# Kernel optimization log

Measured on AMD Instinct MI355X. Metric: run time of the kernel, lower is better.

The kernel has to match this reference:

```python
import math
import jax, jax.numpy as jnp
import numpy as np

B, S, IN_DIM = 4, 2048, 256
L, H, NHEAD, FFN = 3, 256, 4, 1024
CF, CB = 32, 32  # context_forward / context_backward window
EPS = 1e-5


def sinusoidal_pe(seq_len, d_model):
    pos = jnp.arange(seq_len, dtype=jnp.float32)[:, None]
    div = jnp.exp(jnp.arange(0, d_model, 2, dtype=jnp.float32) * (-math.log(10000.0) / d_model))
    pe = jnp.zeros((seq_len, d_model), dtype=jnp.float32)
    pe = pe.at[:, 0::2].set(jnp.sin(pos * div))
    pe = pe.at[:, 1::2].set(jnp.cos(pos * div))
    return pe


def band_mask(s):
    # True = allowed: -CB <= j - i <= CF (sliding window, from triu/transpose construction)
    i = jnp.arange(s)[:, None]
    j = jnp.arange(s)[None, :]
    return (j - i <= CF) & (i - j <= CB)


def layer_norm(x, g, b):
    mu = jnp.mean(x, axis=-1, keepdims=True)
    var = jnp.mean((x - mu) ** 2, axis=-1, keepdims=True)
    return (x - mu) * jax.lax.rsqrt(var + EPS) * g + b


def mha(x, wqkv, bqkv, wo, bo, mask):
    b, s, d = x.shape
    dh = d // NHEAD
    qkv = x @ wqkv.T + bqkv  # [b, s, 3d]
    q, k, v = jnp.split(qkv, 3, axis=-1)
    split = lambda t: t.reshape(b, s, NHEAD, dh).transpose(0, 2, 1, 3)  # [b, h, s, dh]
    q, k, v = split(q), split(k), split(v)
    scores = jnp.einsum('bhqd,bhkd->bhqk', q, k) / math.sqrt(dh)
    scores = jnp.where(mask, scores, -jnp.inf)
    attn = jax.nn.softmax(scores, axis=-1)
    o = jnp.einsum('bhqk,bhkd->bhqd', attn, v).transpose(0, 2, 1, 3).reshape(b, s, d)
    return o @ wo.T + bo


def setup_inputs() -> dict:
    key = jax.random.key(0)
    ks = jax.random.split(key, 12)
    sc = 0.02
    inp = {
        'x': jax.random.normal(ks[0], (B, S, IN_DIM), dtype=jnp.float32),
        'w_in': sc * jax.random.normal(ks[1], (H, IN_DIM), dtype=jnp.float32),
        'w_out': sc * jax.random.normal(ks[2], (IN_DIM, H), dtype=jnp.float32),
        'b_out': jnp.zeros((IN_DIM,), dtype=jnp.float32),
        'qkv_w': sc * jax.random.normal(ks[3], (L, 3 * H, H), dtype=jnp.float32),
        'qkv_b': jnp.zeros((L, 3 * H), dtype=jnp.float32),
        'out_w': sc * jax.random.normal(ks[4], (L, H, H), dtype=jnp.float32),
        'out_b': jnp.zeros((L, H), dtype=jnp.float32),
        'ln1_g': jnp.ones((L, H), dtype=jnp.float32),
        'ln1_b': jnp.zeros((L, H), dtype=jnp.float32),
        'ln2_g': jnp.ones((L, H), dtype=jnp.float32),
        'ln2_b': jnp.zeros((L, H), dtype=jnp.float32),
        'ff1_w': sc * jax.random.normal(ks[5], (L, FFN, H), dtype=jnp.float32),
        'ff1_b': jnp.zeros((L, FFN), dtype=jnp.float32),
        'ff2_w': sc * jax.random.normal(ks[6], (L, H, FFN), dtype=jnp.float32),
        'ff2_b': jnp.zeros((L, H), dtype=jnp.float32),
        'lnf_g': jnp.ones((H,), dtype=jnp.float32),
        'lnf_b': jnp.zeros((H,), dtype=jnp.float32),
    }
    return inp


def reference(x, w_in, w_out, b_out, qkv_w, qkv_b, out_w, out_b,
              ln1_g, ln1_b, ln2_g, ln2_b, ff1_w, ff1_b, ff2_w, ff2_b,
              lnf_g, lnf_b):
    b, s, _ = x.shape
    mask = band_mask(s)
    h = math.sqrt(H) * (x @ w_in.T) + sinusoidal_pe(s, H)[None]
    for l in range(L):  # pre-norm transformer encoder layers (relu FFN, eval/no-dropout)
        h = h + mha(layer_norm(h, ln1_g[l], ln1_b[l]), qkv_w[l], qkv_b[l], out_w[l], out_b[l], mask)
        z = layer_norm(h, ln2_g[l], ln2_b[l])
        h = h + (jax.nn.relu(z @ ff1_w[l].T + ff1_b[l]) @ ff2_w[l].T + ff2_b[l])
    h = layer_norm(h, lnf_g, lnf_b)
    return h @ w_out.T + b_out
```

## Files before the change

kernel.cpp:

```cpp
#include <hip/hip_runtime.h>
#include <hip/hip_bf16.h>
#include <math.h>

#define SEQ 2048
#define BATCH 4
#define HDIM 256
#define NHEAD 4
#define FFN_DIM 1024
#define MTOT (BATCH*SEQ)

typedef __attribute__((ext_vector_type(8))) short bf16x8;
typedef __attribute__((ext_vector_type(4))) float f32x4;

__device__ __forceinline__ bf16x8 cvt8(const float* p)
{
    float4 a = *(const float4*)p;
    float4 b = *(const float4*)(p + 4);
    union { bf16x8 v; __hip_bfloat16 e[8]; } u;
    u.e[0] = __float2bfloat16(a.x); u.e[1] = __float2bfloat16(a.y);
    u.e[2] = __float2bfloat16(a.z); u.e[3] = __float2bfloat16(a.w);
    u.e[4] = __float2bfloat16(b.x); u.e[5] = __float2bfloat16(b.y);
    u.e[6] = __float2bfloat16(b.z); u.e[7] = __float2bfloat16(b.w);
    return u.v;
}

__global__ __launch_bounds__(256)
void cvt_all(const float* __restrict__ w_in, const float* __restrict__ w_out,
             const float* __restrict__ qkv_w, const float* __restrict__ out_w,
             const float* __restrict__ ff1_w, const float* __restrict__ ff2_w,
             __hip_bfloat16* __restrict__ wb)
{
    int i = blockIdx.x * 256 + threadIdx.x;
    size_t e = (size_t)i * 8;

    const float* srcbase; size_t rbase; int kshift;
    if (e < 720896) {
        if (e < 65536)       { srcbase = w_in;  rbase = 0;      kshift = 8; }
        else if (e < 131072) { srcbase = w_out; rbase = 65536;  kshift = 8; }
        else                 { srcbase = qkv_w; rbase = 131072; kshift = 8; }
    } else if (e < 917504)   { srcbase = out_w; rbase = 720896; kshift = 8; }
    else if (e < 1703936)    { srcbase = ff1_w; rbase = 917504; kshift = 8; }
    else                     { srcbase = ff2_w; rbase = 1703936; kshift = 10; }

    size_t local = e - rbase;
    int K = 1 << kshift;
    int row = (int)(local >> kshift);
    int k   = (int)(local & (K - 1));

    size_t dst = rbase
               + ((size_t)(row >> 4) * (K >> 5) + (k >> 5)) * 512
               + (size_t)((((k >> 3) & 3) << 4) | (row & 15)) * 8;

    *(bf16x8*)(wb + dst) = cvt8(srcbase + local);
}

__device__ __forceinline__ bf16x8 fragW(const short* W, int n0, int k0, int K, int lane)
{
    return *(const bf16x8*)(W + ((size_t)(n0 >> 4) * (K >> 5) + (k0 >> 5)) * 512 + lane * 8);
}

__global__ __launch_bounds__(256)
void embed_pe(const float* __restrict__ X, const __hip_bfloat16* __restrict__ W,
              float* __restrict__ hbuf)
{
    int tid = threadIdx.x, wave = tid >> 6, lane = tid & 63;
    int wm = wave >> 1, wn = wave & 1;
    int rowBase = blockIdx.y * 64 + wm * 32;
    int colBase = blockIdx.x * 64 + wn * 32;
    int lr = lane & 15, hi = lane >> 4;

    const float* px0 = X + (size_t)(rowBase + lr) * HDIM + hi * 8;
    const float* px1 = px0 + (size_t)16 * HDIM;
    const short* Wb  = (const short*)W;

    f32x4 acc[2][2];
    acc[0][0] = (f32x4){0.f,0.f,0.f,0.f}; acc[0][1] = (f32x4){0.f,0.f,0.f,0.f};
    acc[1][0] = (f32x4){0.f,0.f,0.f,0.f}; acc[1][1] = (f32x4){0.f,0.f,0.f,0.f};

    #pragma unroll
    for (int k0 = 0; k0 < 256; k0 += 32) {
        bf16x8 a0 = cvt8(px0 + k0);
        bf16x8 a1 = cvt8(px1 + k0);
        bf16x8 b0 = fragW(Wb, colBase,      k0, 256, lane);
        bf16x8 b1 = fragW(Wb, colBase + 16, k0, 256, lane);
        acc[0][0] = __builtin_amdgcn_mfma_f32_16x16x32_bf16(a0, b0, acc[0][0], 0,0,0);
        acc[0][1] = __builtin_amdgcn_mfma_f32_16x16x32_bf16(a0, b1, acc[0][1], 0,0,0);
        acc[1][0] = __builtin_amdgcn_mfma_f32_16x16x32_bf16(a1, b0, acc[1][0], 0,0,0);
        acc[1][1] = __builtin_amdgcn_mfma_f32_16x16x32_bf16(a1, b1, acc[1][1], 0,0,0);
    }

    int cc = lane & 15, quad = lane >> 4;
    #pragma unroll
    for (int mt = 0; mt < 2; mt++)
        #pragma unroll
        for (int nt = 0; nt < 2; nt++) {
            int col = colBase + nt*16 + cc;
            int i2 = col & ~1;
            float freq = __expf((float)i2 * (-9.210340371976184f / 256.0f));
            #pragma unroll
            for (int r = 0; r < 4; r++) {
                int row = rowBase + mt*16 + quad*4 + r;
                float arg = (float)(row & (SEQ-1)) * freq;
                float pe = (col & 1) ? __cosf(arg) : __sinf(arg);
                hbuf[(size_t)row*HDIM + col] = 16.0f*acc[mt][nt][r] + pe;
            }
        }
}

template<int MODE, int NT>
__global__ __launch_bounds__(256)
void gemm_ln(const float* __restrict__ h,
             const float* __restrict__ g, const float* __restrict__ bln,
             const __hip_bfloat16* __restrict__ W,
             const float* __restrict__ bias,
             __hip_bfloat16* __restrict__ obf, float* __restrict__ of32,
             int N, int ldw)
{
    constexpr int NTW = NT / 32;
    __shared__ __align__(16) short A_lds[64][264];

    int tid = threadIdx.x, wave = tid >> 6, lane = tid & 63;
    int wm = wave >> 1, wn = wave & 1;
    int rowBase = blockIdx.y * 64;
    int colBase = blockIdx.x * NT + wn * (NT / 2);

    {
        float4 gv = *(const float4*)(g + lane * 4);
        float4 bv = *(const float4*)(bln + lane * 4);
        #pragma unroll
        for (int rr = 0; rr < 16; rr += 4) {
            float4 xv[4];
            #pragma unroll
            for (int u = 0; u < 4; u++)
                xv[u] = *(const float4*)(h + (size_t)(rowBase + wave*16 + rr + u)*HDIM + lane*4);
            #pragma unroll
            for (int u = 0; u < 4; u++) {
                float s = xv[u].x + xv[u].y + xv[u].z + xv[u].w;
                #pragma unroll
                for (int off = 32; off >= 1; off >>= 1) s += __shfl_xor(s, off);
                float mu = s * (1.0f/256.0f);
                float d0 = xv[u].x-mu, d1 = xv[u].y-mu, d2 = xv[u].z-mu, d3 = xv[u].w-mu;
                float v = d0*d0 + d1*d1 + d2*d2 + d3*d3;
                #pragma unroll
                for (int off = 32; off >= 1; off >>= 1) v += __shfl_xor(v, off);
                float rstd = rsqrtf(v * (1.0f/256.0f) + 1e-5f);
                union { short e[4]; uint2 w2; } o;
                o.e[0] = (short)__bfloat16_as_ushort(__float2bfloat16(d0*rstd*gv.x + bv.x));
                o.e[1] = (short)__bfloat16_as_ushort(__float2bfloat16(d1*rstd*gv.y + bv.y));
                o.e[2] = (short)__bfloat16_as_ushort(__float2bfloat16(d2*rstd*gv.z + bv.z));
                o.e[3] = (short)__bfloat16_as_ushort(__float2bfloat16(d3*rstd*gv.w + bv.w));
                *(uint2*)&A_lds[wave*16 + rr + u][lane*4] = o.w2;
            }
        }
    }
    __syncthreads();

    int lr = lane & 15, hi = lane >> 4;
    f32x4 acc[2][NTW];
    #pragma unroll
    for (int mt = 0; mt < 2; mt++)
        #pragma unroll
        for (int nt = 0; nt < NTW; nt++)
            acc[mt][nt] = (f32x4){0.f,0.f,0.f,0.f};

    const short* Ws = (const short*)W;
    #pragma unroll
    for (int k0 = 0; k0 < 256; k0 += 32) {
        bf16x8 af[2], bfr[NTW];
        #pragma unroll
        for (int mt = 0; mt < 2; mt++)
            af[mt] = *(const bf16x8*)&A_lds[wm*32 + mt*16 + lr][k0 + hi*8];
        #pragma unroll
        for (int nt = 0; nt < NTW; nt++)
            bfr[nt] = fragW(Ws, colBase + nt*16, k0, 256, lane);
        #pragma unroll
        for (int mt = 0; mt < 2; mt++)
            #pragma unroll
            for (int nt = 0; nt < NTW; nt++)
                acc[mt][nt] = __builtin_amdgcn_mfma_f32_16x16x32_bf16(af[mt], bfr[nt], acc[mt][nt], 0,0,0);
    }

    int cc = lane & 15, quad = lane >> 4;
    #pragma unroll
    for (int mt = 0; mt < 2; mt++)
        #pragma unroll
        for (int nt = 0; nt < NTW; nt++) {
            int col = colBase + nt*16 + cc;
            float bv = bias[col];
            #pragma unroll
            for (int r = 0; r < 4; r++) {
                int row = rowBase + wm*32 + mt*16 + quad*4 + r;
                float c = acc[mt][nt][r] + bv;
                if (MODE == 4) { of32[(size_t)row*N + col] = c; }
                else {
                    int sec = col >> 8, hd = (col >> 6) & 3, d = col & 63;
                    int srow = row & (SEQ - 1);
                    size_t base = (size_t)sec * 2097152
                                + (size_t)(((row >> 11) << 2) | hd) * 131072;
                    size_t idx;
                    if (sec < 2)
                        idx = base + (size_t)(srow >> 4) * 1024 + (size_t)(d >> 5) * 512
                            + (size_t)((((d >> 3) & 3) << 4) | (srow & 15)) * 8 + (d & 7);
                    else
                        idx = base + (size_t)srow * 64 + d;
                    obf[idx] = __float2bfloat16(c);
                }
            }
        }
}

struct AttnLDS {
    __align__(16) __hip_bfloat16 Vt[64][128];
    __align__(16) __hip_bfloat16 Pl[32][96];
    float sm[2][32], ss[2][32];
};

__global__ __launch_bounds__(1024)
void attn_ffn(const __hip_bfloat16* __restrict__ qkvd,
              const __hip_bfloat16* __restrict__ ow,
              const float* __restrict__ ob,
              float* __restrict__ h,
              const float* __restrict__ g, const float* __restrict__ bln,
              const __hip_bfloat16* __restrict__ W1, const float* __restrict__ b1,
              const __hip_bfloat16* __restrict__ W2, const float* __restrict__ b2)
{
    __shared__ union SMem {
        AttnLDS asl[4];
        struct {
            __align__(16) short A[32][264];
            __align__(16) short Z[2][32][264];
        } f;
    } U;
    __shared__ __align__(16) short att_lds[32][264];
    __shared__ __align__(16) float H_lds[32][260];

    int tid  = threadIdx.x;
    int wave = tid >> 6, lane = tid & 63;
    int grp  = wave >> 2, w4 = wave & 3, ltid = tid & 255;
    int b    = blockIdx.y, i0 = blockIdx.x * 32;
    int klo  = i0 - 32;

    int lr = lane & 15, hi = lane >> 4;
    int cc = lane & 15, quad = lane >> 4;

    int hd = grp;
    AttnLDS& S = U.asl[grp];
    const short* Qd = (const short*)qkvd + (size_t)(b * 4 + hd) * 131072;
    const short* Kd = Qd + 2097152;
    const short* Vd = Qd + 4194304;
    int qh = w4 & 1, seg = w4 >> 1;
    int qoff = qh * 16 + quad * 4;

    int vm = ltid & 7, vrl = ltid >> 3, vdp = vm * 8;
    bf16x8 vr[3];
    #pragma unroll
    for (int rr = 0; rr < 3; rr++) {
        int j = klo + rr * 32 + vrl;
        j = j < 0 ? 0 : (j > SEQ - 1 ? SEQ - 1 : j);
        vr[rr] = *(const bf16x8*)(Vd + (size_t)j * 64 + vdp);
    }
    bf16x8 qf[2];
    #pragma unroll
    for (int ds = 0; ds < 2; ds++)
        qf[ds] = *(const bf16x8*)(Qd + (size_t)((i0 >> 4) + qh) * 1024 + ds * 512 + lane * 8);
    bf16x8 kf[3][2];
    #pragma unroll
    for (int t = 0; t < 3; t++) {
        int jt = (klo + seg * 48 + t * 16) >> 4;
        jt = jt < 0 ? 0 : (jt > 127 ? 127 : jt);
        kf[t][0] = *(const bf16x8*)(Kd + (size_t)jt * 1024 + lane * 8);
        kf[t][1] = *(const bf16x8*)(Kd + (size_t)jt * 1024 + 512 + lane * 8);
    }
    float hold[2][4];
    {
        const float* hp = h + (size_t)(b * SEQ + i0) * HDIM + wave * 16 + cc;
        #pragma unroll
        for (int mt = 0; mt < 2; mt++)
            #pragma unroll
            for (int r = 0; r < 4; r++)
                hold[mt][r] = hp[(size_t)(mt*16 + quad*4 + r) * HDIM];
    }

    {
        union { bf16x8 v; short e[8]; } u;
        #pragma unroll
        for (int rr = 0; rr < 3; rr++) {
            int row = rr * 32 + vrl;
            int colp = row ^ (vm << 3);
            u.v = vr[rr];
            #pragma unroll
            for (int jj = 0; jj < 8; jj++)
                *(short*)&S.Vt[vdp + jj][colp] = u.e[jj];
        }
    }

    f32x4 sacc[3];
    #pragma unroll
    for (int t = 0; t < 3; t++) {
        f32x4 a = (f32x4){0.f,0.f,0.f,0.f};
        a = __builtin_amdgcn_mfma_f32_16x16x32_bf16(qf[0], kf[t][0], a, 0,0,0);
        a = __builtin_amdgcn_mfma_f32_16x16x32_bf16(qf[1], kf[t][1], a, 0,0,0);
        sacc[t] = a;
    }

    float s[3][4];
    #pragma unroll
    for (int t = 0; t < 3; t++) {
        int koff = seg * 48 + t * 16 + cc;
        int jj = klo + koff;
        #pragma unroll
        for (int r = 0; r < 4; r++) {
            int rel = koff - (qoff + r);
            bool ok = (jj >= 0) && (jj < SEQ) && (rel >= 0) && (rel <= 64);
            s[t][r] = ok ? sacc[t][r] * 0.125f : -1e30f;
        }
    }

    float mrow[4], srow[4];
    #pragma unroll
    for (int r = 0; r < 4; r++)
        mrow[r] = fmaxf(fmaxf(s[0][r], s[1][r]), s[2][r]);
    #pragma unroll
    for (int off = 8; off >= 1; off >>= 1)
        #pragma unroll
        for (int r = 0; r < 4; r++)
            mrow[r] = fmaxf(mrow[r], __shfl_xor(mrow[r], off));
    #pragma unroll
    for (int r = 0; r < 4; r++)
        srow[r] = __expf(s[0][r]-mrow[r]) + __expf(s[1][r]-mrow[r]) + __expf(s[2][r]-mrow[r]);
    #pragma unroll
    for (int off = 8; off >= 1; off >>= 1)
        #pragma unroll
        for (int r = 0; r < 4; r++)
            srow[r] += __shfl_xor(srow[r], off);
    if (cc == 0) {
        #pragma unroll
        for (int r = 0; r < 4; r++) { S.sm[seg][qoff+r] = mrow[r]; S.ss[seg][qoff+r] = srow[r]; }
    }
    __syncthreads();

    float Mr[4], inv[4];
    #pragma unroll
    for (int r = 0; r < 4; r++) {
        float m0 = S.sm[0][qoff+r], m1 = S.sm[1][qoff+r];
        float M = fmaxf(m0, m1);
        float dn = S.ss[0][qoff+r] * __expf(m0 - M) + S.ss[1][qoff+r] * __expf(m1 - M);
        Mr[r] = M; inv[r] = 1.0f / dn;
    }
    #pragma unroll
    for (int t = 0; t < 3; t++)
        #pragma unroll
        for (int r = 0; r < 4; r++)
            S.Pl[qoff+r][seg*48 + t*16 + cc] = __float2bfloat16(__expf(s[t][r]-Mr[r]) * inv[r]);
    __syncthreads();

    bf16x8 owf[8];
    {
        const short* op = (const short*)ow + (size_t)wave * 8 * 512 + lane * 8;
        #pragma unroll
        for (int i = 0; i < 8; i++)
            owf[i] = *(const bf16x8*)(op + i * 512);
    }

    {
        f32x4 oacc[2];
        oacc[0] = (f32x4){0.f,0.f,0.f,0.f}; oacc[1] = (f32x4){0.f,0.f,0.f,0.f};
        #pragma unroll
        for (int ks = 0; ks < 3; ks++) {
            int kk = ks * 32;
            bf16x8 pf = *(const bf16x8*)&S.Pl[qh*16 + lr][kk + hi*8];
            #pragma unroll
            for (int dt = 0; dt < 2; dt++) {
                int d = seg*32 + dt*16 + lr;
                int colb = (kk + hi*8) ^ (((d >> 3) & 7) << 3);
                bf16x8 vf = *(const bf16x8*)&S.Vt[d][colb];
                oacc[dt] = __builtin_amdgcn_mfma_f32_16x16x32_bf16(pf, vf, oacc[dt], 0,0,0);
            }
        }
        #pragma unroll
        for (int dt = 0; dt < 2; dt++) {
            int col = hd*64 + seg*32 + dt*16 + cc;
            #pragma unroll
            for (int r = 0; r < 4; r++)
                att_lds[qoff + r][col] =
                    (short)__bfloat16_as_ushort(__float2bfloat16(oacc[dt][r]));
        }
    }
    __syncthreads();

    {
        f32x4 acc[2];
        acc[0] = (f32x4){0.f,0.f,0.f,0.f}; acc[1] = (f32x4){0.f,0.f,0.f,0.f};
        #pragma unroll
        for (int i = 0; i < 8; i++) {
            bf16x8 a0 = *(const bf16x8*)&att_lds[lr][i*32 + hi*8];
            bf16x8 a1 = *(const bf16x8*)&att_lds[16 + lr][i*32 + hi*8];
            acc[0] = __builtin_amdgcn_mfma_f32_16x16x32_bf16(a0, owf[i], acc[0], 0,0,0);
            acc[1] = __builtin_amdgcn_mfma_f32_16x16x32_bf16(a1, owf[i], acc[1], 0,0,0);
        }
        float bv = ob[wave*16 + cc];
        #pragma unroll
        for (int mt = 0; mt < 2; mt++)
            #pragma unroll
            for (int r = 0; r < 4; r++)
                H_lds[mt*16 + quad*4 + r][wave*16 + cc] = hold[mt][r] + acc[mt][r] + bv;
    }

    const short* W1s = (const short*)W1;
    const short* W2s = (const short*)W2;
    bf16x8 w1f[8];
    {
        const short* wp = W1s + (size_t)wave * 8 * 512 + lane * 8;
        #pragma unroll
        for (int i = 0; i < 8; i++)
            w1f[i] = *(const bf16x8*)(wp + i * 512);
    }
    __syncthreads();

    {
        float4 gv = *(const float4*)(g + lane * 4);
        float4 bv = *(const float4*)(bln + lane * 4);
        #pragma unroll
        for (int u = 0; u < 2; u++) {
            float4 xv = *(const float4*)&H_lds[wave*2 + u][lane*4];
            float ss2 = xv.x + xv.y + xv.z + xv.w;
            #pragma unroll
            for (int off = 32; off >= 1; off >>= 1) ss2 += __shfl_xor(ss2, off);
            float mu = ss2 * (1.0f/256.0f);
            float d0 = xv.x-mu, d1 = xv.y-mu, d2 = xv.z-mu, d3 = xv.w-mu;
            float v = d0*d0 + d1*d1 + d2*d2 + d3*d3;
            #pragma unroll
            for (int off = 32; off >= 1; off >>= 1) v += __shfl_xor(v, off);
            float rstd = rsqrtf(v * (1.0f/256.0f) + 1e-5f);
            union { short e[4]; uint2 w2; } o;
            o.e[0] = (short)__bfloat16_as_ushort(__float2bfloat16(d0*rstd*gv.x + bv.x));
            o.e[1] = (short)__bfloat16_as_ushort(__float2bfloat16(d1*rstd*gv.y + bv.y));
            o.e[2] = (short)__bfloat16_as_ushort(__float2bfloat16(d2*rstd*gv.z + bv.z));
            o.e[3] = (short)__bfloat16_as_ushort(__float2bfloat16(d3*rstd*gv.w + bv.w));
            *(uint2*)&U.f.A[wave*2 + u][lane*4] = o.w2;
        }
    }
    __syncthreads();

    f32x4 acc2[2];
    acc2[0] = (f32x4){0.f,0.f,0.f,0.f}; acc2[1] = (f32x4){0.f,0.f,0.f,0.f};

    #pragma unroll 1
    for (int kk = 0; kk < 4; kk++) {
        bf16x8 w2f[8];
        {
            const short* wp = W2s + (size_t)(wave * 32 + kk * 8) * 512 + lane * 8;
            #pragma unroll
            for (int i = 0; i < 8; i++)
                w2f[i] = *(const bf16x8*)(wp + i * 512);
        }

        f32x4 acc1[2];
        acc1[0] = (f32x4){0.f,0.f,0.f,0.f}; acc1[1] = (f32x4){0.f,0.f,0.f,0.f};
        #pragma unroll
        for (int i = 0; i < 8; i++) {
            bf16x8 af0 = *(const bf16x8*)&U.f.A[lr][i*32 + hi*8];
            bf16x8 af1 = *(const bf16x8*)&U.f.A[16 + lr][i*32 + hi*8];
            acc1[0] = __builtin_amdgcn_mfma_f32_16x16x32_bf16(af0, w1f[i], acc1[0], 0,0,0);
            acc1[1] = __builtin_amdgcn_mfma_f32_16x16x32_bf16(af1, w1f[i], acc1[1], 0,0,0);
        }

        {
            int col = wave*16 + cc;
            float bb = b1[kk*256 + col];
            #pragma unroll
            for (int mt = 0; mt < 2; mt++)
                #pragma unroll
                for (int r = 0; r < 4; r++) {
                    float z = fmaxf(acc1[mt][r] + bb, 0.f);
                    U.f.Z[kk & 1][mt*16 + quad*4 + r][col] =
                        (short)__bfloat16_as_ushort(__float2bfloat16(z));
                }
        }
        __syncthreads();

        {
            int nk = (kk < 3) ? kk + 1 : 3;
            const short* wp = W1s + (size_t)(nk * 16 + wave) * 8 * 512 + lane * 8;
            #pragma unroll
            for (int i = 0; i < 8; i++)
                w1f[i] = *(const bf16x8*)(wp + i * 512);
        }

        #pragma unroll
        for (int i = 0; i < 8; i++) {
            bf16x8 zf0 = *(const bf16x8*)&U.f.Z[kk & 1][lr][i*32 + hi*8];
            bf16x8 zf1 = *(const bf16x8*)&U.f.Z[kk & 1][16 + lr][i*32 + hi*8];
            acc2[0] = __builtin_amdgcn_mfma_f32_16x16x32_bf16(zf0, w2f[i], acc2[0], 0,0,0);
            acc2[1] = __builtin_amdgcn_mfma_f32_16x16x32_bf16(zf1, w2f[i], acc2[1], 0,0,0);
        }
    }

    {
        int col = wave*16 + cc;
        float bb = b2[col];
        #pragma unroll
        for (int mt = 0; mt < 2; mt++)
            #pragma unroll
            for (int r = 0; r < 4; r++) {
                int rowl = mt*16 + quad*4 + r;
                int row = b * SEQ + i0 + rowl;
                h[(size_t)row * HDIM + col] = H_lds[rowl][col] + acc2[mt][r] + bb;
            }
    }
}

extern "C" void kernel_launch(void* const* d_in, const int* in_sizes, int n_in,
                              void* d_out, int out_size, void* d_ws, size_t ws_size,
                              hipStream_t stream)
{
    const float* x     = (const float*)d_in[0];
    const float* w_in  = (const float*)d_in[1];
    const float* w_out = (const float*)d_in[2];
    const float* b_out = (const float*)d_in[3];
    const float* qkv_w = (const float*)d_in[4];
    const float* qkv_b = (const float*)d_in[5];
    const float* out_w = (const float*)d_in[6];
    const float* out_b = (const float*)d_in[7];
    const float* ln1_g = (const float*)d_in[8];
    const float* ln1_b = (const float*)d_in[9];
    const float* ln2_g = (const float*)d_in[10];
    const float* ln2_b = (const float*)d_in[11];
    const float* ff1_w = (const float*)d_in[12];
    const float* ff1_b = (const float*)d_in[13];
    const float* ff2_w = (const float*)d_in[14];
    const float* ff2_b = (const float*)d_in[15];
    const float* lnf_g = (const float*)d_in[16];
    const float* lnf_b = (const float*)d_in[17];

    char* ws = (char*)d_ws;
    float*          h    = (float*)ws;
    __hip_bfloat16* qkvd = (__hip_bfloat16*)(ws + 8388608);
    __hip_bfloat16* wb   = (__hip_bfloat16*)(ws + 25165824);

    __hip_bfloat16* w_in_b  = wb;
    __hip_bfloat16* w_out_b = wb + 65536;
    __hip_bfloat16* qkv_w_b = wb + 131072;
    __hip_bfloat16* out_w_b = wb + 720896;
    __hip_bfloat16* ff1_w_b = wb + 917504;
    __hip_bfloat16* ff2_w_b = wb + 1703936;

    dim3 blk(256);

    cvt_all<<<1216, blk, 0, stream>>>(w_in, w_out, qkv_w, out_w, ff1_w, ff2_w, wb);

    embed_pe<<<dim3(4, 128), blk, 0, stream>>>(x, w_in_b, h);

    for (int l = 0; l < 3; l++) {
        gemm_ln<5, 96><<<dim3(8, 128), blk, 0, stream>>>(
            h, ln1_g + l*HDIM, ln1_b + l*HDIM,
            qkv_w_b + (size_t)l*768*HDIM, qkv_b + l*768, qkvd, nullptr, 768, HDIM);
        attn_ffn<<<dim3(SEQ/32, BATCH), dim3(1024), 0, stream>>>(
            qkvd, out_w_b + (size_t)l*HDIM*HDIM, out_b + l*HDIM, h,
            ln2_g + l*HDIM, ln2_b + l*HDIM,
            ff1_w_b + (size_t)l*FFN_DIM*HDIM, ff1_b + l*FFN_DIM,
            ff2_w_b + (size_t)l*HDIM*FFN_DIM, ff2_b + l*HDIM);
    }

    gemm_ln<4, 64><<<dim3(4, 128), blk, 0, stream>>>(
        h, lnf_g, lnf_b, w_out_b, b_out, nullptr, (float*)d_out, HDIM, HDIM);
}
```

Measured before the change: 252.5 us.

## Fuse whole encoder into one cooperative persistent kernel with grid syncs

Replaces the embed, per-layer QKV GEMM, attention/FFN and final projection launches with one cooperative kernel. Each 32-row block keeps its residual stream in LDS for all layers, and grid.sync separates QKV production from the attention that reads neighbouring rows' K/V. QKV buffers are double-buffered so the next layer's QKV write does not overwrite data other blocks are still reading. This removes launch overhead and the global round trips of h. The cost is grid-wide barriers and a requirement that all 256 blocks of 1024 threads are co-resident.

```diff
diff --git a/kernel.cpp b/kernel.cpp
--- a/kernel.cpp
+++ b/kernel.cpp
@@ -1,6 +1,9 @@
 #include <hip/hip_runtime.h>
 #include <hip/hip_bf16.h>
+#include <hip/hip_cooperative_groups.h>
 #include <math.h>
+
+namespace cg = cooperative_groups;
 
 #define SEQ 2048
 #define BATCH 4
@@ -59,154 +62,44 @@
     return *(const bf16x8*)(W + ((size_t)(n0 >> 4) * (K >> 5) + (k0 >> 5)) * 512 + lane * 8);
 }
 
-__global__ __launch_bounds__(256)
-void embed_pe(const float* __restrict__ X, const __hip_bfloat16* __restrict__ W,
-              float* __restrict__ hbuf)
-{
-    int tid = threadIdx.x, wave = tid >> 6, lane = tid & 63;
-    int wm = wave >> 1, wn = wave & 1;
-    int rowBase = blockIdx.y * 64 + wm * 32;
-    int colBase = blockIdx.x * 64 + wn * 32;
-    int lr = lane & 15, hi = lane >> 4;
-
-    const float* px0 = X + (size_t)(rowBase + lr) * HDIM + hi * 8;
-    const float* px1 = px0 + (size_t)16 * HDIM;
-    const short* Wb  = (const short*)W;
-
-    f32x4 acc[2][2];
-    acc[0][0] = (f32x4){0.f,0.f,0.f,0.f}; acc[0][1] = (f32x4){0.f,0.f,0.f,0.f};
-    acc[1][0] = (f32x4){0.f,0.f,0.f,0.f}; acc[1][1] = (f32x4){0.f,0.f,0.f,0.f};
-
+__device__ __forceinline__ size_t qkv_idx(int row, int col)
+{
+    int sec = col >> 8, hd = (col >> 6) & 3, d = col & 63;
+    int srow = row & (SEQ - 1);
+    size_t base = (size_t)sec * 2097152
+                + (size_t)(((row >> 11) << 2) | hd) * 131072;
+    if (sec < 2)
+        return base + (size_t)(srow >> 4) * 1024 + (size_t)(d >> 5) * 512
+             + (size_t)((((d >> 3) & 3) << 4) | (srow & 15)) * 8 + (d & 7);
+    return base + (size_t)srow * 64 + d;
+}
+
+__device__ __forceinline__ void ln_rows(const float (*H)[260], short (*A)[264],
+                                        const float* __restrict__ g,
+                                        const float* __restrict__ bl,
+                                        int wave, int lane)
+{
+    float4 gv = *(const float4*)(g + lane * 4);
+    float4 bv = *(const float4*)(bl + lane * 4);
     #pragma unroll
-    for (int k0 = 0; k0 < 256; k0 += 32) {
-        bf16x8 a0 = cvt8(px0 + k0);
-        bf16x8 a1 = cvt8(px1 + k0);
-        bf16x8 b0 = fragW(Wb, colBase,      k0, 256, lane);
-        bf16x8 b1 = fragW(Wb, colBase + 16, k0, 256, lane);
-        acc[0][0] = __builtin_amdgcn_mfma_f32_16x16x32_bf16(a0, b0, acc[0][0], 0,0,0);
-        acc[0][1] = __builtin_amdgcn_mfma_f32_16x16x32_bf16(a0, b1, acc[0][1], 0,0,0);
-        acc[1][0] = __builtin_amdgcn_mfma_f32_16x16x32_bf16(a1, b0, acc[1][0], 0,0,0);
-        acc[1][1] = __builtin_amdgcn_mfma_f32_16x16x32_bf16(a1, b1, acc[1][1], 0,0,0);
+    for (int u = 0; u < 2; u++) {
+        float4 xv = *(const float4*)&H[wave*2 + u][lane*4];
+        float ss2 = xv.x + xv.y + xv.z + xv.w;
+        #pragma unroll
+        for (int off = 32; off >= 1; off >>= 1) ss2 += __shfl_xor(ss2, off);
+        float mu = ss2 * (1.0f/256.0f);
+        float d0 = xv.x-mu, d1 = xv.y-mu, d2 = xv.z-mu, d3 = xv.w-mu;
+        float v = d0*d0 + d1*d1 + d2*d2 + d3*d3;
+        #pragma unroll
+        for (int off = 32; off >= 1; off >>= 1) v += __shfl_xor(v, off);
+        float rstd = rsqrtf(v * (1.0f/256.0f) + 1e-5f);
+        union { short e[4]; uint2 w2; } o;
+        o.e[0] = (short)__bfloat16_as_ushort(__float2bfloat16(d0*rstd*gv.x + bv.x));
+        o.e[1] = (short)__bfloat16_as_ushort(__float2bfloat16(d1*rstd*gv.y + bv.y));
+        o.e[2] = (short)__bfloat16_as_ushort(__float2bfloat16(d2*rstd*gv.z + bv.z));
+        o.e[3] = (short)__bfloat16_as_ushort(__float2bfloat16(d3*rstd*gv.w + bv.w));
+        *(uint2*)&A[wave*2 + u][lane*4] = o.w2;
     }
-
-    int cc = lane & 15, quad = lane >> 4;
-    #pragma unroll
-    for (int mt = 0; mt < 2; mt++)
-        #pragma unroll
-        for (int nt = 0; nt < 2; nt++) {
-            int col = colBase + nt*16 + cc;
-            int i2 = col & ~1;
-            float freq = __expf((float)i2 * (-9.210340371976184f / 256.0f));
-            #pragma unroll
-            for (int r = 0; r < 4; r++) {
-                int row = rowBase + mt*16 + quad*4 + r;
-                float arg = (float)(row & (SEQ-1)) * freq;
-                float pe = (col & 1) ? __cosf(arg) : __sinf(arg);
-                hbuf[(size_t)row*HDIM + col] = 16.0f*acc[mt][nt][r] + pe;
-            }
-        }
-}
-
-template<int MODE, int NT>
-__global__ __launch_bounds__(256)
-void gemm_ln(const float* __restrict__ h,
-             const float* __restrict__ g, const float* __restrict__ bln,
-             const __hip_bfloat16* __restrict__ W,
-             const float* __restrict__ bias,
-             __hip_bfloat16* __restrict__ obf, float* __restrict__ of32,
-             int N, int ldw)
-{
-    constexpr int NTW = NT / 32;
-    __shared__ __align__(16) short A_lds[64][264];
-
-    int tid = threadIdx.x, wave = tid >> 6, lane = tid & 63;
-    int wm = wave >> 1, wn = wave & 1;
-    int rowBase = blockIdx.y * 64;
-    int colBase = blockIdx.x * NT + wn * (NT / 2);
-
-    {
-        float4 gv = *(const float4*)(g + lane * 4);
-        float4 bv = *(const float4*)(bln + lane * 4);
-        #pragma unroll
-        for (int rr = 0; rr < 16; rr += 4) {
-            float4 xv[4];
-            #pragma unroll
-            for (int u = 0; u < 4; u++)
-                xv[u] = *(const float4*)(h + (size_t)(rowBase + wave*16 + rr + u)*HDIM + lane*4);
-            #pragma unroll
-            for (int u = 0; u < 4; u++) {
-                float s = xv[u].x + xv[u].y + xv[u].z + xv[u].w;
-                #pragma unroll
-                for (int off = 32; off >= 1; off >>= 1) s += __shfl_xor(s, off);
-                float mu = s * (1.0f/256.0f);
-                float d0 = xv[u].x-mu, d1 = xv[u].y-mu, d2 = xv[u].z-mu, d3 = xv[u].w-mu;
-                float v = d0*d0 + d1*d1 + d2*d2 + d3*d3;
-                #pragma unroll
-                for (int off = 32; off >= 1; off >>= 1) v += __shfl_xor(v, off);
-                float rstd = rsqrtf(v * (1.0f/256.0f) + 1e-5f);
-                union { short e[4]; uint2 w2; } o;
-                o.e[0] = (short)__bfloat16_as_ushort(__float2bfloat16(d0*rstd*gv.x + bv.x));
-                o.e[1] = (short)__bfloat16_as_ushort(__float2bfloat16(d1*rstd*gv.y + bv.y));
-                o.e[2] = (short)__bfloat16_as_ushort(__float2bfloat16(d2*rstd*gv.z + bv.z));
-                o.e[3] = (short)__bfloat16_as_ushort(__float2bfloat16(d3*rstd*gv.w + bv.w));
-                *(uint2*)&A_lds[wave*16 + rr + u][lane*4] = o.w2;
-            }
-        }
-    }
-    __syncthreads();
-
-    int lr = lane & 15, hi = lane >> 4;
-    f32x4 acc[2][NTW];
-    #pragma unroll
-    for (int mt = 0; mt < 2; mt++)
-        #pragma unroll
-        for (int nt = 0; nt < NTW; nt++)
-            acc[mt][nt] = (f32x4){0.f,0.f,0.f,0.f};
-
-    const short* Ws = (const short*)W;
-    #pragma unroll
-    for (int k0 = 0; k0 < 256; k0 += 32) {
-        bf16x8 af[2], bfr[NTW];
-        #pragma unroll
-        for (int mt = 0; mt < 2; mt++)
-            af[mt] = *(const bf16x8*)&A_lds[wm*32 + mt*16 + lr][k0 + hi*8];
-        #pragma unroll
-        for (int nt = 0; nt < NTW; nt++)
-            bfr[nt] = fragW(Ws, colBase + nt*16, k0, 256, lane);
-        #pragma unroll
-        for (int mt = 0; mt < 2; mt++)
-            #pragma unroll
-            for (int nt = 0; nt < NTW; nt++)
-                acc[mt][nt] = __builtin_amdgcn_mfma_f32_16x16x32_bf16(af[mt], bfr[nt], acc[mt][nt], 0,0,0);
-    }
-
-    int cc = lane & 15, quad = lane >> 4;
-    #pragma unroll
-    for (int mt = 0; mt < 2; mt++)
-        #pragma unroll
-        for (int nt = 0; nt < NTW; nt++) {
-            int col = colBase + nt*16 + cc;
-            float bv = bias[col];
-            #pragma unroll
-            for (int r = 0; r < 4; r++) {
-                int row = rowBase + wm*32 + mt*16 + quad*4 + r;
-                float c = acc[mt][nt][r] + bv;
-                if (MODE == 4) { of32[(size_t)row*N + col] = c; }
-                else {
-                    int sec = col >> 8, hd = (col >> 6) & 3, d = col & 63;
-                    int srow = row & (SEQ - 1);
-                    size_t base = (size_t)sec * 2097152
-                                + (size_t)(((row >> 11) << 2) | hd) * 131072;
-                    size_t idx;
-                    if (sec < 2)
-                        idx = base + (size_t)(srow >> 4) * 1024 + (size_t)(d >> 5) * 512
-                            + (size_t)((((d >> 3) & 3) << 4) | (srow & 15)) * 8 + (d & 7);
-                    else
-                        idx = base + (size_t)srow * 64 + d;
-                    obf[idx] = __float2bfloat16(c);
-                }
-            }
-        }
 }
 
 struct AttnLDS {
@@ -216,13 +109,18 @@
 };
 
 __global__ __launch_bounds__(1024)
-void attn_ffn(const __hip_bfloat16* __restrict__ qkvd,
-              const __hip_bfloat16* __restrict__ ow,
-              const float* __restrict__ ob,
-              float* __restrict__ h,
-              const float* __restrict__ g, const float* __restrict__ bln,
-              const __hip_bfloat16* __restrict__ W1, const float* __restrict__ b1,
-              const __hip_bfloat16* __restrict__ W2, const float* __restrict__ b2)
+void mega(const float* __restrict__ X,
+          const __hip_bfloat16* __restrict__ wb,
+          const float* __restrict__ qkv_b,
+          const float* __restrict__ out_b,
+          const float* __restrict__ ln1_g, const float* __restrict__ ln1_b,
+          const float* __restrict__ ln2_g, const float* __restrict__ ln2_b,
+          const float* __restrict__ ff1_b, const float* __restrict__ ff2_b,
+          const float* __restrict__ lnf_g, const float* __restrict__ lnf_b,
+          const float* __restrict__ b_out,
+          float* __restrict__ outp,
+          __hip_bfloat16* __restrict__ qkvd0,
+          __hip_bfloat16* __restrict__ qkvd1)
 {
     __shared__ union SMem {
         AttnLDS asl[4];
@@ -234,6 +132,8 @@
     __shared__ __align__(16) short att_lds[32][264];
     __shared__ __align__(16) float H_lds[32][260];
 
+    cg::grid_group grid = cg::this_grid();
+
     int tid  = threadIdx.x;
     int wave = tid >> 6, lane = tid & 63;
     int grp  = wave >> 2, w4 = wave & 3, ltid = tid & 255;
@@ -242,271 +142,386 @@
 
     int lr = lane & 15, hi = lane >> 4;
     int cc = lane & 15, quad = lane >> 4;
-
-    int hd = grp;
-    AttnLDS& S = U.asl[grp];
-    const short* Qd = (const short*)qkvd + (size_t)(b * 4 + hd) * 131072;
-    const short* Kd = Qd + 2097152;
-    const short* Vd = Qd + 4194304;
     int qh = w4 & 1, seg = w4 >> 1;
     int qoff = qh * 16 + quad * 4;
 
-    int vm = ltid & 7, vrl = ltid >> 3, vdp = vm * 8;
-    bf16x8 vr[3];
-    #pragma unroll
-    for (int rr = 0; rr < 3; rr++) {
-        int j = klo + rr * 32 + vrl;
-        j = j < 0 ? 0 : (j > SEQ - 1 ? SEQ - 1 : j);
-        vr[rr] = *(const bf16x8*)(Vd + (size_t)j * 64 + vdp);
-    }
-    bf16x8 qf[2];
-    #pragma unroll
-    for (int ds = 0; ds < 2; ds++)
-        qf[ds] = *(const bf16x8*)(Qd + (size_t)((i0 >> 4) + qh) * 1024 + ds * 512 + lane * 8);
-    bf16x8 kf[3][2];
-    #pragma unroll
-    for (int t = 0; t < 3; t++) {
-        int jt = (klo + seg * 48 + t * 16) >> 4;
-        jt = jt < 0 ? 0 : (jt > 127 ? 127 : jt);
-        kf[t][0] = *(const bf16x8*)(Kd + (size_t)jt * 1024 + lane * 8);
-        kf[t][1] = *(const bf16x8*)(Kd + (size_t)jt * 1024 + 512 + lane * 8);
-    }
-    float hold[2][4];
+    const short* wbs = (const short*)wb;
+
     {
-        const float* hp = h + (size_t)(b * SEQ + i0) * HDIM + wave * 16 + cc;
+        const float* px0 = X + (size_t)(b*SEQ + i0 + lr) * HDIM + hi * 8;
+        const float* px1 = px0 + (size_t)16 * HDIM;
+        f32x4 acc[2];
+        acc[0] = (f32x4){0.f,0.f,0.f,0.f}; acc[1] = (f32x4){0.f,0.f,0.f,0.f};
+        #pragma unroll
+        for (int k0 = 0; k0 < 256; k0 += 32) {
+            bf16x8 a0 = cvt8(px0 + k0);
+            bf16x8 a1 = cvt8(px1 + k0);
+            bf16x8 b0 = fragW(wbs, wave*16, k0, 256, lane);
+            acc[0] = __builtin_amdgcn_mfma_f32_16x16x32_bf16(a0, b0, acc[0], 0,0,0);
+            acc[1] = __builtin_amdgcn_mfma_f32_16x16x32_bf16(a1, b0, acc[1], 0,0,0);
+        }
+        int col = wave*16 + cc;
+        int i2 = col & ~1;
+        float freq = __expf((float)i2 * (-9.210340371976184f / 256.0f));
         #pragma unroll
         for (int mt = 0; mt < 2; mt++)
             #pragma unroll
-            for (int r = 0; r < 4; r++)
-                hold[mt][r] = hp[(size_t)(mt*16 + quad*4 + r) * HDIM];
-    }
-
-    {
-        union { bf16x8 v; short e[8]; } u;
-        #pragma unroll
-        for (int rr = 0; rr < 3; rr++) {
-            int row = rr * 32 + vrl;
-            int colp = row ^ (vm << 3);
-            u.v = vr[rr];
-            #pragma unroll
-            for (int jj = 0; jj < 8; jj++)
-                *(short*)&S.Vt[vdp + jj][colp] = u.e[jj];
-        }
-    }
-
-    f32x4 sacc[3];
-    #pragma unroll
-    for (int t = 0; t < 3; t++) {
-        f32x4 a = (f32x4){0.f,0.f,0.f,0.f};
-        a = __builtin_amdgcn_mfma_f32_16x16x32_bf16(qf[0], kf[t][0], a, 0,0,0);
-        a = __builtin_amdgcn_mfma_f32_16x16x32_bf16(qf[1], kf[t][1], a, 0,0,0);
-        sacc[t] = a;
-    }
-
-    float s[3][4];
-    #pragma unroll
-    for (int t = 0; t < 3; t++) {
-        int koff = seg * 48 + t * 16 + cc;
-        int jj = klo + koff;
-        #pragma unroll
-        for (int r = 0; r < 4; r++) {
-            int rel = koff - (qoff + r);
-            bool ok = (jj >= 0) && (jj < SEQ) && (rel >= 0) && (rel <= 64);
-            s[t][r] = ok ? sacc[t][r] * 0.125f : -1e30f;
-        }
-    }
-
-    float mrow[4], srow[4];
-    #pragma unroll
-    for (int r = 0; r < 4; r++)
-        mrow[r] = fmaxf(fmaxf(s[0][r], s[1][r]), s[2][r]);
-    #pragma unroll
-    for (int off = 8; off >= 1; off >>= 1)
-        #pragma unroll
-        for (int r = 0; r < 4; r++)
-            mrow[r] = fmaxf(mrow[r], __shfl_xor(mrow[r], off));
-    #pragma unroll
-    for (int r = 0; r < 4; r++)
-        srow[r] = __expf(s[0][r]-mrow[r]) + __expf(s[1][r]-mrow[r]) + __expf(s[2][r]-mrow[r]);
-    #pragma unroll
-    for (int off = 8; off >= 1; off >>= 1)
-        #pragma unroll
-        for (int r = 0; r < 4; r++)
-            srow[r] += __shfl_xor(srow[r], off);
-    if (cc == 0) {
-        #pragma unroll
-        for (int r = 0; r < 4; r++) { S.sm[seg][qoff+r] = mrow[r]; S.ss[seg][qoff+r] = srow[r]; }
+            for (int r = 0; r < 4; r++) {
+                int srow = i0 + mt*16 + quad*4 + r;
+                float arg = (float)srow * freq;
+                float pe = (col & 1) ? __cosf(arg) : __sinf(arg);
+                H_lds[mt*16 + quad*4 + r][col] = 16.0f*acc[mt][r] + pe;
+            }
     }
     __syncthreads();
 
-    float Mr[4], inv[4];
-    #pragma unroll
-    for (int r = 0; r < 4; r++) {
-        float m0 = S.sm[0][qoff+r], m1 = S.sm[1][qoff+r];
-        float M = fmaxf(m0, m1);
-        float dn = S.ss[0][qoff+r] * __expf(m0 - M) + S.ss[1][qoff+r] * __expf(m1 - M);
-        Mr[r] = M; inv[r] = 1.0f / dn;
+    ln_rows(H_lds, U.f.A, ln1_g, ln1_b, wave, lane);
+    __syncthreads();
+    {
+        const short* Wts = wbs + 131072;
+        f32x4 qa[2][3];
+        #pragma unroll
+        for (int mt = 0; mt < 2; mt++)
+            #pragma unroll
+            for (int nt = 0; nt < 3; nt++)
+                qa[mt][nt] = (f32x4){0.f,0.f,0.f,0.f};
+        #pragma unroll
+        for (int k0 = 0; k0 < 256; k0 += 32) {
+            bf16x8 a0 = *(const bf16x8*)&U.f.A[lr][k0 + hi*8];
+            bf16x8 a1 = *(const bf16x8*)&U.f.A[16 + lr][k0 + hi*8];
+            #pragma unroll
+            for (int nt = 0; nt < 3; nt++) {
+                bf16x8 wf = fragW(Wts, wave*48 + nt*16, k0, 256, lane);
+                qa[0][nt] = __builtin_amdgcn_mfma_f32_16x16x32_bf16(a0, wf, qa[0][nt], 0,0,0);
+                qa[1][nt] = __builtin_amdgcn_mfma_f32_16x16x32_bf16(a1, wf, qa[1][nt], 0,0,0);
+            }
+        }
+        #pragma unroll
+        for (int nt = 0; nt < 3; nt++) {
+            int col = wave*48 + nt*16 + cc;
+            float bv = qkv_b[col];
+            #pragma unroll
+            for (int mt = 0; mt < 2; mt++)
+                #pragma unroll
+                for (int r = 0; r < 4; r++) {
+                    int row = b * SEQ + i0 + mt*16 + quad*4 + r;
+                    qkvd0[qkv_idx(row, col)] = __float2bfloat16(qa[mt][nt][r] + bv);
+                }
+        }
     }
-    #pragma unroll
-    for (int t = 0; t < 3; t++)
+    __threadfence();
+    grid.sync();
+
+    #pragma unroll 1
+    for (int l = 0; l < 3; l++) {
+        const short* Qbase = (const short*)((l == 1) ? qkvd1 : qkvd0);
+        const short* ows = wbs + 720896 + (size_t)l * 65536;
+        const short* W1s = wbs + 917504 + (size_t)l * 262144;
+        const short* W2s = wbs + 1703936 + (size_t)l * 262144;
+        const float* ob  = out_b + l * HDIM;
+        const float* b1  = ff1_b + l * FFN_DIM;
+        const float* b2  = ff2_b + l * HDIM;
+        const float* g2  = ln2_g + l * HDIM;
+        const float* bl2 = ln2_b + l * HDIM;
+
+        int hd = grp;
+        AttnLDS& S = U.asl[grp];
+        const short* Qd = Qbase + (size_t)(b * 4 + hd) * 131072;
+        const short* Kd = Qd + 2097152;
+        const short* Vd = Qd + 4194304;
+
+        int vm = ltid & 7, vrl = ltid >> 3, vdp = vm * 8;
+        bf16x8 vr[3];
+        #pragma unroll
+        for (int rr = 0; rr < 3; rr++) {
+            int j = klo + rr * 32 + vrl;
+            j = j < 0 ? 0 : (j > SEQ - 1 ? SEQ - 1 : j);
+            vr[rr] = *(const bf16x8*)(Vd + (size_t)j * 64 + vdp);
+        }
+        bf16x8 qf[2];
+        #pragma unroll
+        for (int ds = 0; ds < 2; ds++)
+            qf[ds] = *(const bf16x8*)(Qd + (size_t)((i0 >> 4) + qh) * 1024 + ds * 512 + lane * 8);
+        bf16x8 kf[3][2];
+        #pragma unroll
+        for (int t = 0; t < 3; t++) {
+            int jt = (klo + seg * 48 + t * 16) >> 4;
+            jt = jt < 0 ? 0 : (jt > 127 ? 127 : jt);
+            kf[t][0] = *(const bf16x8*)(Kd + (size_t)jt * 1024 + lane * 8);
+            kf[t][1] = *(const bf16x8*)(Kd + (size_t)jt * 1024 + 512 + lane * 8);
+        }
+
+        {
+            union { bf16x8 v; short e[8]; } u;
+            #pragma unroll
+            for (int rr = 0; rr < 3; rr++) {
+                int row = rr * 32 + vrl;
+                int colp = row ^ (vm << 3);
+                u.v = vr[rr];
+                #pragma unroll
+                for (int jj = 0; jj < 8; jj++)
+                    *(short*)&S.Vt[vdp + jj][colp] = u.e[jj];
+            }
+        }
+
+        f32x4 sacc[3];
+        #pragma unroll
+        for (int t = 0; t < 3; t++) {
+            f32x4 a = (f32x4){0.f,0.f,0.f,0.f};
+            a = __builtin_amdgcn_mfma_f32_16x16x32_bf16(qf[0], kf[t][0], a, 0,0,0);
+            a = __builtin_amdgcn_mfma_f32_16x16x32_bf16(qf[1], kf[t][1], a, 0,0,0);
+            sacc[t] = a;
+        }
+
+        float s[3][4];
+        #pragma unroll
+        for (int t = 0; t < 3; t++) {
+            int koff = seg * 48 + t * 16 + cc;
+            int jj = klo + koff;
+            #pragma unroll
+            for (int r = 0; r < 4; r++) {
+                int rel = koff - (qoff + r);
+                bool ok = (jj >= 0) && (jj < SEQ) && (rel >= 0) && (rel <= 64);
+                s[t][r] = ok ? sacc[t][r] * 0.125f : -1e30f;
+            }
+        }
+
+        float mrow[4], srow[4];
         #pragma unroll
         for (int r = 0; r < 4; r++)
-            S.Pl[qoff+r][seg*48 + t*16 + cc] = __float2bfloat16(__expf(s[t][r]-Mr[r]) * inv[r]);
-    __syncthreads();
-
-    bf16x8 owf[8];
-    {
-        const short* op = (const short*)ow + (size_t)wave * 8 * 512 + lane * 8;
-        #pragma unroll
-        for (int i = 0; i < 8; i++)
-            owf[i] = *(const bf16x8*)(op + i * 512);
-    }
-
-    {
-        f32x4 oacc[2];
-        oacc[0] = (f32x4){0.f,0.f,0.f,0.f}; oacc[1] = (f32x4){0.f,0.f,0.f,0.f};
-        #pragma unroll
-        for (int ks = 0; ks < 3; ks++) {
-            int kk = ks * 32;
-            bf16x8 pf = *(const bf16x8*)&S.Pl[qh*16 + lr][kk + hi*8];
+            mrow[r] = fmaxf(fmaxf(s[0][r], s[1][r]), s[2][r]);
+        #pragma unroll
+        for (int off = 8; off >= 1; off >>= 1)
+            #pragma unroll
+            for (int r = 0; r < 4; r++)
+                mrow[r] = fmaxf(mrow[r], __shfl_xor(mrow[r], off));
+        #pragma unroll
+        for (int r = 0; r < 4; r++)
+            srow[r] = __expf(s[0][r]-mrow[r]) + __expf(s[1][r]-mrow[r]) + __expf(s[2][r]-mrow[r]);
+        #pragma unroll
+        for (int off = 8; off >= 1; off >>= 1)
+            #pragma unroll
+            for (int r = 0; r < 4; r++)
+                srow[r] += __shfl_xor(srow[r], off);
+        if (cc == 0) {
+            #pragma unroll
+            for (int r = 0; r < 4; r++) { S.sm[seg][qoff+r] = mrow[r]; S.ss[seg][qoff+r] = srow[r]; }
+        }
+        __syncthreads();
+
+        float Mr[4], inv[4];
+        #pragma unroll
+        for (int r = 0; r < 4; r++) {
+            float m0 = S.sm[0][qoff+r], m1 = S.sm[1][qoff+r];
+            float M = fmaxf(m0, m1);
+            float dn = S.ss[0][qoff+r] * __expf(m0 - M) + S.ss[1][qoff+r] * __expf(m1 - M);
+            Mr[r] = M; inv[r] = 1.0f / dn;
+        }
+        #pragma unroll
+        for (int t = 0; t < 3; t++)
+            #pragma unroll
+            for (int r = 0; r < 4; r++)
+                S.Pl[qoff+r][seg*48 + t*16 + cc] = __float2bfloat16(__expf(s[t][r]-Mr[r]) * inv[r]);
+        __syncthreads();
+
+        bf16x8 owf[8];
+        {
+            const short* op = ows + (size_t)wave * 8 * 512 + lane * 8;
+            #pragma unroll
+            for (int i = 0; i < 8; i++)
+                owf[i] = *(const bf16x8*)(op + i * 512);
+        }
+
+        {
+            f32x4 oacc[2];
+            oacc[0] = (f32x4){0.f,0.f,0.f,0.f}; oacc[1] = (f32x4){0.f,0.f,0.f,0.f};
+            #pragma unroll
+            for (int ks = 0; ks < 3; ks++) {
+                int kk = ks * 32;
+                bf16x8 pf = *(const bf16x8*)&S.Pl[qh*16 + lr][kk + hi*8];
+                #pragma unroll
+                for (int dt = 0; dt < 2; dt++) {
+                    int d = seg*32 + dt*16 + lr;
+                    int colb = (kk + hi*8) ^ (((d >> 3) & 7) << 3);
+                    bf16x8 vf = *(const bf16x8*)&S.Vt[d][colb];
+                    oacc[dt] = __builtin_amdgcn_mfma_f32_16x16x32_bf16(pf, vf, oacc[dt], 0,0,0);
+                }
+            }
             #pragma unroll
             for (int dt = 0; dt < 2; dt++) {
-                int d = seg*32 + dt*16 + lr;
-                int colb = (kk + hi*8) ^ (((d >> 3) & 7) << 3);
-                bf16x8 vf = *(const bf16x8*)&S.Vt[d][colb];
-                oacc[dt] = __builtin_amdgcn_mfma_f32_16x16x32_bf16(pf, vf, oacc[dt], 0,0,0);
-            }
-        }
-        #pragma unroll
-        for (int dt = 0; dt < 2; dt++) {
-            int col = hd*64 + seg*32 + dt*16 + cc;
-            #pragma unroll
-            for (int r = 0; r < 4; r++)
-                att_lds[qoff + r][col] =
-                    (short)__bfloat16_as_ushort(__float2bfloat16(oacc[dt][r]));
-        }
-    }
-    __syncthreads();
-
-    {
-        f32x4 acc[2];
-        acc[0] = (f32x4){0.f,0.f,0.f,0.f}; acc[1] = (f32x4){0.f,0.f,0.f,0.f};
-        #pragma unroll
-        for (int i = 0; i < 8; i++) {
-            bf16x8 a0 = *(const bf16x8*)&att_lds[lr][i*32 + hi*8];
-            bf16x8 a1 = *(const bf16x8*)&att_lds[16 + lr][i*32 + hi*8];
-            acc[0] = __builtin_amdgcn_mfma_f32_16x16x32_bf16(a0, owf[i], acc[0], 0,0,0);
-            acc[1] = __builtin_amdgcn_mfma_f32_16x16x32_bf16(a1, owf[i], acc[1], 0,0,0);
-        }
-        float bv = ob[wave*16 + cc];
-        #pragma unroll
-        for (int mt = 0; mt < 2; mt++)
-            #pragma unroll
-            for (int r = 0; r < 4; r++)
-                H_lds[mt*16 + quad*4 + r][wave*16 + cc] = hold[mt][r] + acc[mt][r] + bv;
-    }
-
-    const short* W1s = (const short*)W1;
-    const short* W2s = (const short*)W2;
-    bf16x8 w1f[8];
-    {
-        const short* wp = W1s + (size_t)wave * 8 * 512 + lane * 8;
-        #pragma unroll
-        for (int i = 0; i < 8; i++)
-            w1f[i] = *(const bf16x8*)(wp + i * 512);
-    }
-    __syncthreads();
-
-    {
-        float4 gv = *(const float4*)(g + lane * 4);
-        float4 bv = *(const float4*)(bln + lane * 4);
-        #pragma unroll
-        for (int u = 0; u < 2; u++) {
-            float4 xv = *(const float4*)&H_lds[wave*2 + u][lane*4];
-            float ss2 = xv.x + xv.y + xv.z + xv.w;
-            #pragma unroll
-            for (int off = 32; off >= 1; off >>= 1) ss2 += __shfl_xor(ss2, off);
-            float mu = ss2 * (1.0f/256.0f);
-            float d0 = xv.x-mu, d1 = xv.y-mu, d2 = xv.z-mu, d3 = xv.w-mu;
-            float v = d0*d0 + d1*d1 + d2*d2 + d3*d3;
-            #pragma unroll
-            for (int off = 32; off >= 1; off >>= 1) v += __shfl_xor(v, off);
-            float rstd = rsqrtf(v * (1.0f/256.0f) + 1e-5f);
-            union { short e[4]; uint2 w2; } o;
-            o.e[0] = (short)__bfloat16_as_ushort(__float2bfloat16(d0*rstd*gv.x + bv.x));
-            o.e[1] = (short)__bfloat16_as_ushort(__float2bfloat16(d1*rstd*gv.y + bv.y));
-            o.e[2] = (short)__bfloat16_as_ushort(__float2bfloat16(d2*rstd*gv.z + bv.z));
-            o.e[3] = (short)__bfloat16_as_ushort(__float2bfloat16(d3*rstd*gv.w + bv.w));
-            *(uint2*)&U.f.A[wave*2 + u][lane*4] = o.w2;
-        }
-    }
-    __syncthreads();
-
-    f32x4 acc2[2];
-    acc2[0] = (f32x4){0.f,0.f,0.f,0.f}; acc2[1] = (f32x4){0.f,0.f,0.f,0.f};
-
-    #pragma unroll 1
-    for (int kk = 0; kk < 4; kk++) {
-        bf16x8 w2f[8];
+                int col = hd*64 + seg*32 + dt*16 + cc;
+                #pragma unroll
+                for (int r = 0; r < 4; r++)
+                    att_lds[qoff + r][col] =
+                        (short)__bfloat16_as_ushort(__float2bfloat16(oacc[dt][r]));
+            }
+        }
+        __syncthreads();
+
         {
-            const short* wp = W2s + (size_t)(wave * 32 + kk * 8) * 512 + lane * 8;
+            f32x4 acc[2];
+            acc[0] = (f32x4){0.f,0.f,0.f,0.f}; acc[1] = (f32x4){0.f,0.f,0.f,0.f};
+            #pragma unroll
+            for (int i = 0; i < 8; i++) {
+                bf16x8 a0 = *(const bf16x8*)&att_lds[lr][i*32 + hi*8];
+                bf16x8 a1 = *(const bf16x8*)&att_lds[16 + lr][i*32 + hi*8];
+                acc[0] = __builtin_amdgcn_mfma_f32_16x16x32_bf16(a0, owf[i], acc[0], 0,0,0);
+                acc[1] = __builtin_amdgcn_mfma_f32_16x16x32_bf16(a1, owf[i], acc[1], 0,0,0);
+            }
+            float bv = ob[wave*16 + cc];
+            #pragma unroll
+            for (int mt = 0; mt < 2; mt++)
+                #pragma unroll
+                for (int r = 0; r < 4; r++)
+                    H_lds[mt*16 + quad*4 + r][wave*16 + cc] += acc[mt][r] + bv;
+        }
+
+        bf16x8 w1f[8];
+        {
+            const short* wp = W1s + (size_t)wave * 8 * 512 + lane * 8;
             #pragma unroll
             for (int i = 0; i < 8; i++)
-                w2f[i] = *(const bf16x8*)(wp + i * 512);
-        }
-
-        f32x4 acc1[2];
-        acc1[0] = (f32x4){0.f,0.f,0.f,0.f}; acc1[1] = (f32x4){0.f,0.f,0.f,0.f};
-        #pragma unroll
-        for (int i = 0; i < 8; i++) {
-            bf16x8 af0 = *(const bf16x8*)&U.f.A[lr][i*32 + hi*8];
-            bf16x8 af1 = *(const bf16x8*)&U.f.A[16 + lr][i*32 + hi*8];
-            acc1[0] = __builtin_amdgcn_mfma_f32_16x16x32_bf16(af0, w1f[i], acc1[0], 0,0,0);
-            acc1[1] = __builtin_amdgcn_mfma_f32_16x16x32_bf16(af1, w1f[i], acc1[1], 0,0,0);
+                w1f[i] = *(const bf16x8*)(wp + i * 512);
+        }
+        __syncthreads();
+
+        ln_rows(H_lds, U.f.A, g2, bl2, wave, lane);
+        __syncthreads();
+
+        f32x4 acc2[2];
+        acc2[0] = (f32x4){0.f,0.f,0.f,0.f}; acc2[1] = (f32x4){0.f,0.f,0.f,0.f};
+
+        #pragma unroll 1
+        for (int kk = 0; kk < 4; kk++) {
+            bf16x8 w2f[8];
+            {
+                const short* wp = W2s + (size_t)(wave * 32 + kk * 8) * 512 + lane * 8;
+                #pragma unroll
+                for (int i = 0; i < 8; i++)
+                    w2f[i] = *(const bf16x8*)(wp + i * 512);
+            }
+
+            f32x4 acc1[2];
+            acc1[0] = (f32x4){0.f,0.f,0.f,0.f}; acc1[1] = (f32x4){0.f,0.f,0.f,0.f};
+            #pragma unroll
+            for (int i = 0; i < 8; i++) {
+                bf16x8 af0 = *(const bf16x8*)&U.f.A[lr][i*32 + hi*8];
+                bf16x8 af1 = *(const bf16x8*)&U.f.A[16 + lr][i*32 + hi*8];
+                acc1[0] = __builtin_amdgcn_mfma_f32_16x16x32_bf16(af0, w1f[i], acc1[0], 0,0,0);
+                acc1[1] = __builtin_amdgcn_mfma_f32_16x16x32_bf16(af1, w1f[i], acc1[1], 0,0,0);
+            }
+
+            {
+                int col = wave*16 + cc;
+                float bb = b1[kk*256 + col];
+                #pragma unroll
+                for (int mt = 0; mt < 2; mt++)
+                    #pragma unroll
+                    for (int r = 0; r < 4; r++) {
+                        float z = fmaxf(acc1[mt][r] + bb, 0.f);
+                        U.f.Z[kk & 1][mt*16 + quad*4 + r][col] =
+                            (short)__bfloat16_as_ushort(__float2bfloat16(z));
+                    }
+            }
+            __syncthreads();
+
+            {
+                int nk = (kk < 3) ? kk + 1 : 3;
+                const short* wp = W1s + (size_t)(nk * 16 + wave) * 8 * 512 + lane * 8;
+                #pragma unroll
+                for (int i = 0; i < 8; i++)
+                    w1f[i] = *(const bf16x8*)(wp + i * 512);
+            }
+
+            #pragma unroll
+            for (int i = 0; i < 8; i++) {
+                bf16x8 zf0 = *(const bf16x8*)&U.f.Z[kk & 1][lr][i*32 + hi*8];
+                bf16x8 zf1 = *(const bf16x8*)&U.f.Z[kk & 1][16 + lr][i*32 + hi*8];
+                acc2[0] = __builtin_amdgcn_mfma_f32_16x16x32_bf16(zf0, w2f[i], acc2[0], 0,0,0);
+                acc2[1] = __builtin_amdgcn_mfma_f32_16x16x32_bf16(zf1, w2f[i], acc2[1], 0,0,0);
+            }
         }
 
         {
             int col = wave*16 + cc;
-            float bb = b1[kk*256 + col];
+            float bb = b2[col];
             #pragma unroll
             for (int mt = 0; mt < 2; mt++)
                 #pragma unroll
                 for (int r = 0; r < 4; r++) {
-                    float z = fmaxf(acc1[mt][r] + bb, 0.f);
-                    U.f.Z[kk & 1][mt*16 + quad*4 + r][col] =
-                        (short)__bfloat16_as_ushort(__float2bfloat16(z));
+                    int rowl = mt*16 + quad*4 + r;
+                    H_lds[rowl][col] = H_lds[rowl][col] + acc2[mt][r] + bb;
                 }
         }
         __syncthreads();
 
-        {
-            int nk = (kk < 3) ? kk + 1 : 3;
-            const short* wp = W1s + (size_t)(nk * 16 + wave) * 8 * 512 + lane * 8;
+        const float* gt = (l < 2) ? (ln1_g + (l+1)*HDIM) : lnf_g;
+        const float* bt = (l < 2) ? (ln1_b + (l+1)*HDIM) : lnf_b;
+        ln_rows(H_lds, U.f.A, gt, bt, wave, lane);
+        __syncthreads();
+
+        if (l < 2) {
+            const short* Wts = wbs + 131072 + (size_t)(l+1) * 196608;
+            const float* btb = qkv_b + (l+1) * 768;
+            __hip_bfloat16* qdst = (l == 0) ? qkvd1 : qkvd0;
+
+            f32x4 qa[2][3];
+            #pragma unroll
+            for (int mt = 0; mt < 2; mt++)
+                #pragma unroll
+                for (int nt = 0; nt < 3; nt++)
+                    qa[mt][nt] = (f32x4){0.f,0.f,0.f,0.f};
+            #pragma unroll
+            for (int k0 = 0; k0 < 256; k0 += 32) {
+                bf16x8 a0 = *(const bf16x8*)&U.f.A[lr][k0 + hi*8];
+                bf16x8 a1 = *(const bf16x8*)&U.f.A[16 + lr][k0 + hi*8];
+                #pragma unroll
+                for (int nt = 0; nt < 3; nt++) {
+                    bf16x8 wf = fragW(Wts, wave*48 + nt*16, k0, 256, lane);
+                    qa[0][nt] = __builtin_amdgcn_mfma_f32_16x16x32_bf16(a0, wf, qa[0][nt], 0,0,0);
+                    qa[1][nt] = __builtin_amdgcn_mfma_f32_16x16x32_bf16(a1, wf, qa[1][nt], 0,0,0);
+                }
+            }
+            #pragma unroll
+            for (int nt = 0; nt < 3; nt++) {
+                int col = wave*48 + nt*16 + cc;
+                float bv = btb[col];
+                #pragma unroll
+                for (int mt = 0; mt < 2; mt++)
+                    #pragma unroll
+                    for (int r = 0; r < 4; r++) {
+                        int row = b * SEQ + i0 + mt*16 + quad*4 + r;
+                        qdst[qkv_idx(row, col)] = __float2bfloat16(qa[mt][nt][r] + bv);
+                    }
+            }
+            __threadfence();
+            grid.sync();
+        } else {
+            bf16x8 wf[8];
+            const short* wp = wbs + 65536 + (size_t)wave * 8 * 512 + lane * 8;
             #pragma unroll
             for (int i = 0; i < 8; i++)
-                w1f[i] = *(const bf16x8*)(wp + i * 512);
-        }
-
-        #pragma unroll
-        for (int i = 0; i < 8; i++) {
-            bf16x8 zf0 = *(const bf16x8*)&U.f.Z[kk & 1][lr][i*32 + hi*8];
-            bf16x8 zf1 = *(const bf16x8*)&U.f.Z[kk & 1][16 + lr][i*32 + hi*8];
-            acc2[0] = __builtin_amdgcn_mfma_f32_16x16x32_bf16(zf0, w2f[i], acc2[0], 0,0,0);
-            acc2[1] = __builtin_amdgcn_mfma_f32_16x16x32_bf16(zf1, w2f[i], acc2[1], 0,0,0);
-        }
-    }
-
-    {
-        int col = wave*16 + cc;
-        float bb = b2[col];
-        #pragma unroll
-        for (int mt = 0; mt < 2; mt++)
-            #pragma unroll
-            for (int r = 0; r < 4; r++) {
-                int rowl = mt*16 + quad*4 + r;
-                int row = b * SEQ + i0 + rowl;
-                h[(size_t)row * HDIM + col] = H_lds[rowl][col] + acc2[mt][r] + bb;
-            }
+                wf[i] = *(const bf16x8*)(wp + i * 512);
+
+            f32x4 oa[2];
+            oa[0] = (f32x4){0.f,0.f,0.f,0.f}; oa[1] = (f32x4){0.f,0.f,0.f,0.f};
+            #pragma unroll
+            for (int i = 0; i < 8; i++) {
+                bf16x8 a0 = *(const bf16x8*)&U.f.A[lr][i*32 + hi*8];
+                bf16x8 a1 = *(const bf16x8*)&U.f.A[16 + lr][i*32 + hi*8];
+                oa[0] = __builtin_amdgcn_mfma_f32_16x16x32_bf16(a0, wf[i], oa[0], 0,0,0);
+                oa[1] = __builtin_amdgcn_mfma_f32_16x16x32_bf16(a1, wf[i], oa[1], 0,0,0);
+            }
+            int col = wave*16 + cc;
+            float bb = b_out[col];
+            #pragma unroll
+            for (int mt = 0; mt < 2; mt++)
+                #pragma unroll
+                for (int r = 0; r < 4; r++) {
+                    int row = b * SEQ + i0 + mt*16 + quad*4 + r;
+                    outp[(size_t)row * HDIM + col] = oa[mt][r] + bb;
+                }
+        }
     }
 }
 
@@ -534,34 +549,25 @@
     const float* lnf_b = (const float*)d_in[17];
 
     char* ws = (char*)d_ws;
-    float*          h    = (float*)ws;
-    __hip_bfloat16* qkvd = (__hip_bfloat16*)(ws + 8388608);
-    __hip_bfloat16* wb   = (__hip_bfloat16*)(ws + 25165824);
-
-    __hip_bfloat16* w_in_b  = wb;
-    __hip_bfloat16* w_out_b = wb + 65536;
-    __hip_bfloat16* qkv_w_b = wb + 131072;
-    __hip_bfloat16* out_w_b = wb + 720896;
-    __hip_bfloat16* ff1_w_b = wb + 917504;
-    __hip_bfloat16* ff2_w_b = wb + 1703936;
-
-    dim3 blk(256);
-
-    cvt_all<<<1216, blk, 0, stream>>>(w_in, w_out, qkv_w, out_w, ff1_w, ff2_w, wb);
-
-    embed_pe<<<dim3(4, 128), blk, 0, stream>>>(x, w_in_b, h);
-
-    for (int l = 0; l < 3; l++) {
-        gemm_ln<5, 96><<<dim3(8, 128), blk, 0, stream>>>(
-            h, ln1_g + l*HDIM, ln1_b + l*HDIM,
-            qkv_w_b + (size_t)l*768*HDIM, qkv_b + l*768, qkvd, nullptr, 768, HDIM);
-        attn_ffn<<<dim3(SEQ/32, BATCH), dim3(1024), 0, stream>>>(
-            qkvd, out_w_b + (size_t)l*HDIM*HDIM, out_b + l*HDIM, h,
-            ln2_g + l*HDIM, ln2_b + l*HDIM,
-            ff1_w_b + (size_t)l*FFN_DIM*HDIM, ff1_b + l*FFN_DIM,
-            ff2_w_b + (size_t)l*HDIM*FFN_DIM, ff2_b + l*HDIM);
-    }
-
-    gemm_ln<4, 64><<<dim3(4, 128), blk, 0, stream>>>(
-        h, lnf_g, lnf_b, w_out_b, b_out, nullptr, (float*)d_out, HDIM, HDIM);
-}
+    __hip_bfloat16* qkvd0 = (__hip_bfloat16*)ws;
+    __hip_bfloat16* qkvd1 = (__hip_bfloat16*)(ws + 12582912);
+    __hip_bfloat16* wb    = (__hip_bfloat16*)(ws + 25165824);
+
+    cvt_all<<<1216, dim3(256), 0, stream>>>(w_in, w_out, qkv_w, out_w, ff1_w, ff2_w, wb);
+
+    const float* Xp = x;
+    const __hip_bfloat16* wbp = wb;
+    float* outp = (float*)d_out;
+    void* args[] = {
+        (void*)&Xp, (void*)&wbp,
+        (void*)&qkv_b, (void*)&out_b,
+        (void*)&ln1_g, (void*)&ln1_b,
+        (void*)&ln2_g, (void*)&ln2_b,
+        (void*)&ff1_b, (void*)&ff2_b,
+        (void*)&lnf_g, (void*)&lnf_b,
+        (void*)&b_out, (void*)&outp,
+        (void*)&qkvd0, (void*)&qkvd1,
+    };
+    hipLaunchCooperativeKernel((const void*)mega, dim3(SEQ/32, BATCH), dim3(1024),
+                               args, 0, stream);
+}
```

New measurement: 690.8 us. 2.74x slower.
